# Performance work log

Measured on AMD Instinct MI355X. Metric: run time of the kernel, lower is better.

The kernel has to match this reference:

```python
import jax, jax.numpy as jnp
import numpy as np

# Production-scale dims
B = 256        # graphs per batch
NPG = 500      # nodes per graph (equal-size graphs; k<=NPG so no padding branch)
N = B * NPG    # 128000 total nodes
F = 128        # num_node_feats
D = 32         # latent_dim
K = 30         # sort-pool k
L = 3          # num_layers
E = 2_048_000  # edges (avg degree 16)


def _mlp(x, wa, ba, wb, bb):
    # 2-layer MLP(in -> D -> D) with ReLU between layers (standard GIN-style MLP)
    return jax.nn.relu(x @ wa + ba) @ wb + bb


def setup_inputs() -> dict:
    key = jax.random.key(0)
    ks = jax.random.split(key, 10)
    s = 0.05
    return {
        "node_feat": jax.random.normal(ks[0], (N, F), jnp.float32),
        "alpha": jax.random.normal(ks[1], (L + 1,), jnp.float32) * 0.5,
        "w0a": jax.random.normal(ks[2], (F, D), jnp.float32) * s,
        "b0a": jnp.zeros((D,), jnp.float32),
        "w0b": jax.random.normal(ks[3], (D, D), jnp.float32) * s,
        "b0b": jnp.zeros((D,), jnp.float32),
        "W1a": jax.random.normal(ks[4], (L, 3 * D, D), jnp.float32) * s,
        "B1a": jnp.zeros((L, D), jnp.float32),
        "W1b": jax.random.normal(ks[5], (L, D, D), jnp.float32) * s,
        "B1b": jnp.zeros((L, D), jnp.float32),
        "edge_src": jax.random.randint(ks[6], (E,), 0, N, jnp.int32),
        "edge_dst": jax.random.randint(ks[7], (E,), 0, N, jnp.int32),
    }


def reference(node_feat, alpha, w0a, b0a, w0b, b0b, W1a, B1a, W1b, B1b,
              edge_src, edge_dst):
    # --- aggregate_combine ---
    ego = _mlp(node_feat, w0a, b0a, w0b, b0b)            # [N, D]
    out = alpha[0] * ego
    for l in range(L):
        # gnn_spmm(n2n_sp, ego): binary adjacency SpMM == scatter-add over edges
        neig = jax.ops.segment_sum(ego[edge_src], edge_dst, num_segments=N)  # [N, D]
        agg = jnp.concatenate([ego, neig, neig + ego], axis=1)               # [N, 3D]
        ego = _mlp(agg, W1a[l], B1a[l], W1b[l], B1b[l])                      # [N, D]
        out = out + alpha[l + 1] * ego
    # --- per-graph sort pooling on wl_color = last channel of final ego ---
    wl_color = ego[:, -1].reshape(B, NPG)                # [B, NPG]
    _, idx = jax.lax.top_k(wl_color, K)                  # [B, K] local indices
    gidx = (idx + jnp.arange(B, dtype=idx.dtype)[:, None] * NPG).reshape(-1)
    sort_graphs = out[gidx].reshape(B, K * D)            # [B, k*latent_dim]
    return jax.nn.relu(sort_graphs)
```

## Files before the change

kernel.cpp:

```cpp
#include <hip/hip_runtime.h>
#include <math.h>

#define N_NODES 128000
#define B_G 256
#define NPG 500
#define F_IN 128
#define D_LAT 32
#define K_TOP 30
#define L_LAYERS 3
#define E_EDGES 2048000

#define BSH 7
#define NB (N_NODES >> BSH)
#define CHUNK 8192
#define CBLOCKS (E_EDGES / CHUNK)

__global__ __launch_bounds__(256) void k_mlp0(
    const float* __restrict__ X, const float* __restrict__ w0a,
    const float* __restrict__ b0a, const float* __restrict__ w0b,
    const float* __restrict__ b0b, const float* __restrict__ alpha,
    float* __restrict__ ego, float* __restrict__ outb)
{
    __shared__ float sWa[F_IN * D_LAT];
    __shared__ float sWb[D_LAT * D_LAT];
    __shared__ float sBa[D_LAT], sBb[D_LAT];

    const int t = threadIdx.x;
    for (int i = t; i < F_IN * D_LAT / 4; i += 256)
        ((float4*)sWa)[i] = ((const float4*)w0a)[i];
    for (int i = t; i < D_LAT * D_LAT / 4; i += 256)
        ((float4*)sWb)[i] = ((const float4*)w0b)[i];
    if (t < D_LAT) { sBa[t] = b0a[t]; sBb[t] = b0b[t]; }

    const size_t row = (size_t)blockIdx.x * 256 + t;
    const float4* xp = (const float4*)(X + row * F_IN);
    const float a0 = alpha[0];
    __syncthreads();

    float acc[D_LAT];
    #pragma unroll
    for (int d = 0; d < D_LAT; ++d) acc[d] = sBa[d];

    #pragma unroll
    for (int c = 0; c < F_IN / 16; ++c) {
        float4 x4[4];
        #pragma unroll
        for (int q = 0; q < 4; ++q) x4[q] = xp[c * 4 + q];
        #pragma unroll
        for (int q = 0; q < 4; ++q) {
            const float xs[4] = {x4[q].x, x4[q].y, x4[q].z, x4[q].w};
            #pragma unroll
            for (int ff = 0; ff < 4; ++ff) {
                const float xf = xs[ff];
                const float4* wr = (const float4*)(sWa + (c * 16 + q * 4 + ff) * D_LAT);
                #pragma unroll
                for (int dq = 0; dq < D_LAT / 4; ++dq) {
                    const float4 w = wr[dq];
                    acc[dq * 4 + 0] = fmaf(xf, w.x, acc[dq * 4 + 0]);
                    acc[dq * 4 + 1] = fmaf(xf, w.y, acc[dq * 4 + 1]);
                    acc[dq * 4 + 2] = fmaf(xf, w.z, acc[dq * 4 + 2]);
                    acc[dq * 4 + 3] = fmaf(xf, w.w, acc[dq * 4 + 3]);
                }
            }
        }
    }

    float acc2[D_LAT];
    #pragma unroll
    for (int d = 0; d < D_LAT; ++d) acc2[d] = sBb[d];
    #pragma unroll
    for (int dd = 0; dd < D_LAT; ++dd) {
        const float h = fmaxf(acc[dd], 0.f);
        const float4* wr = (const float4*)(sWb + dd * D_LAT);
        #pragma unroll
        for (int dq = 0; dq < D_LAT / 4; ++dq) {
            const float4 w = wr[dq];
            acc2[dq * 4 + 0] = fmaf(h, w.x, acc2[dq * 4 + 0]);
            acc2[dq * 4 + 1] = fmaf(h, w.y, acc2[dq * 4 + 1]);
            acc2[dq * 4 + 2] = fmaf(h, w.z, acc2[dq * 4 + 2]);
            acc2[dq * 4 + 3] = fmaf(h, w.w, acc2[dq * 4 + 3]);
        }
    }

    float4* eo = (float4*)(ego + row * D_LAT);
    float4* oo = (float4*)(outb + row * D_LAT);
    #pragma unroll
    for (int dq = 0; dq < D_LAT / 4; ++dq) {
        eo[dq] = make_float4(acc2[dq*4], acc2[dq*4+1], acc2[dq*4+2], acc2[dq*4+3]);
        oo[dq] = make_float4(a0*acc2[dq*4], a0*acc2[dq*4+1], a0*acc2[dq*4+2], a0*acc2[dq*4+3]);
    }
}

__global__ __launch_bounds__(256) void k_bcount(
    const int* __restrict__ edst, int* __restrict__ ghist)
{
    __shared__ int cnt[NB];
    const int t = threadIdx.x;
    for (int i = t; i < NB; i += 256) cnt[i] = 0;
    __syncthreads();
    const int ebase = blockIdx.x * CHUNK;
    for (int i = 0; i < CHUNK / 256; ++i)
        atomicAdd(&cnt[edst[ebase + i * 256 + t] >> BSH], 1);
    __syncthreads();
    for (int i = t; i < NB; i += 256)
        if (cnt[i]) atomicAdd(&ghist[i], cnt[i]);
}

__global__ __launch_bounds__(1024) void k_bscan(
    const int* __restrict__ ghist, int* __restrict__ gbase,
    int* __restrict__ gcursor)
{
    __shared__ int buf[2][1024];
    const int t = threadIdx.x;
    const int v = (t < NB) ? ghist[t] : 0;
    buf[0][t] = v;
    __syncthreads();
    int cur = 0;
    for (int o = 1; o < 1024; o <<= 1) {
        int x = buf[cur][t];
        if (t >= o) x += buf[cur][t - o];
        buf[cur ^ 1][t] = x;
        cur ^= 1;
        __syncthreads();
    }
    if (t < NB) { const int e = buf[cur][t] - v; gbase[t] = e; gcursor[t] = e; }
    if (t == 0) gbase[NB] = E_EDGES;
}

__global__ __launch_bounds__(256) void k_bscatter(
    const int* __restrict__ esrc, const int* __restrict__ edst,
    int* __restrict__ gcursor, int* __restrict__ packed)
{
    __shared__ int cnt[NB];
    __shared__ int sbase[NB];
    const int t = threadIdx.x;
    for (int i = t; i < NB; i += 256) cnt[i] = 0;
    __syncthreads();
    const int ebase = blockIdx.x * CHUNK;
    for (int i = 0; i < CHUNK / 256; ++i)
        atomicAdd(&cnt[edst[ebase + i * 256 + t] >> BSH], 1);
    __syncthreads();
    for (int i = t; i < NB; i += 256) {
        const int c = cnt[i];
        sbase[i] = c ? atomicAdd(&gcursor[i], c) : 0;
        cnt[i] = 0;
    }
    __syncthreads();
    for (int i = 0; i < CHUNK / 256; ++i) {
        const int e = ebase + i * 256 + t;
        const int d = edst[e], s = esrc[e];
        const int b = d >> BSH;
        const int r = atomicAdd(&cnt[b], 1);
        packed[sbase[b] + r] = (s << BSH) | (d & ((1 << BSH) - 1));
    }
}

__global__ __launch_bounds__(256) void k_bcsr(
    const int* __restrict__ gbase, const int* __restrict__ packed,
    int* __restrict__ off, int* __restrict__ srcidx)
{
    __shared__ int cnt[128];
    __shared__ int scn[128];
    __shared__ int sbuf[4096];
    const int b = blockIdx.x, t = threadIdx.x;
    const int s0 = gbase[b], s1 = gbase[b + 1], m = s1 - s0;

    if (t < 128) cnt[t] = 0;
    __syncthreads();
    for (int i = t; i < m; i += 256)
        atomicAdd(&cnt[packed[s0 + i] & 127], 1);
    __syncthreads();
    if (t == 0) {
        int a = 0;
        for (int k = 0; k < 128; ++k) { scn[k] = a; a += cnt[k]; }
    }
    __syncthreads();
    if (t < 128) { off[(b << BSH) + t] = s0 + scn[t]; cnt[t] = 0; }
    if (b == 0 && t == 0) off[N_NODES] = E_EDGES;
    __syncthreads();
    for (int i = t; i < m; i += 256) {
        const int p = packed[s0 + i];
        const int dl = p & 127;
        const int r = atomicAdd(&cnt[dl], 1);
        sbuf[scn[dl] + r] = p >> BSH;
    }
    __syncthreads();
    for (int i = t; i < m; i += 256) srcidx[s0 + i] = sbuf[i];
}

__global__ __launch_bounds__(256) void k_gather(
    const float* __restrict__ ego, const int* __restrict__ off,
    const int* __restrict__ srcidx, float* __restrict__ neig)
{
    const int t = threadIdx.x;
    const int node = blockIdx.x * 32 + (t >> 3);
    const int c = (t & 7) * 4;
    const int s0 = off[node], s1 = off[node + 1];
    float4 acc = {0.f, 0.f, 0.f, 0.f};
    for (int i = s0; i < s1; ++i) {
        const int s = srcidx[i];
        const float4 v = *(const float4*)(ego + (size_t)s * D_LAT + c);
        acc.x += v.x; acc.y += v.y; acc.z += v.z; acc.w += v.w;
    }
    *(float4*)(neig + (size_t)node * D_LAT + c) = acc;
}

__global__ __launch_bounds__(256) void k_mlp1(
    const float* __restrict__ ego_in, const float* __restrict__ neig,
    const float* __restrict__ W1a_l, const float* __restrict__ B1a_l,
    const float* __restrict__ W1b_l, const float* __restrict__ B1b_l,
    const float* __restrict__ alpha, const int l,
    float* __restrict__ ego_out, float* __restrict__ outb)
{
    __shared__ float sWe[D_LAT * D_LAT], sWn[D_LAT * D_LAT], sWb[D_LAT * D_LAT];
    __shared__ float sBa[D_LAT], sBb[D_LAT];

    const int t = threadIdx.x;
    for (int i = t; i < D_LAT * D_LAT; i += 256) {
        const float wc = W1a_l[2 * D_LAT * D_LAT + i];
        sWe[i] = W1a_l[i] + wc;
        sWn[i] = W1a_l[D_LAT * D_LAT + i] + wc;
        sWb[i] = W1b_l[i];
    }
    if (t < D_LAT) { sBa[t] = B1a_l[t]; sBb[t] = B1b_l[t]; }

    const size_t row = (size_t)blockIdx.x * 256 + t;
    const float4* ep = (const float4*)(ego_in + row * D_LAT);
    const float4* np_ = (const float4*)(neig + row * D_LAT);
    const float al = alpha[l + 1];
    __syncthreads();

    float acc[D_LAT];
    #pragma unroll
    for (int d = 0; d < D_LAT; ++d) acc[d] = sBa[d];

    #pragma unroll
    for (int c = 0; c < D_LAT / 4; ++c) {
        const float4 e4 = ep[c];
        const float4 n4 = np_[c];
        const float es[4] = {e4.x, e4.y, e4.z, e4.w};
        const float ns[4] = {n4.x, n4.y, n4.z, n4.w};
        #pragma unroll
        for (int ff = 0; ff < 4; ++ff) {
            const float fe = es[ff], fn = ns[ff];
            const float4* we = (const float4*)(sWe + (c * 4 + ff) * D_LAT);
            const float4* wn = (const float4*)(sWn + (c * 4 + ff) * D_LAT);
            #pragma unroll
            for (int dq = 0; dq < D_LAT / 4; ++dq) {
                const float4 a = we[dq], b = wn[dq];
                acc[dq * 4 + 0] = fmaf(fe, a.x, fmaf(fn, b.x, acc[dq * 4 + 0]));
                acc[dq * 4 + 1] = fmaf(fe, a.y, fmaf(fn, b.y, acc[dq * 4 + 1]));
                acc[dq * 4 + 2] = fmaf(fe, a.z, fmaf(fn, b.z, acc[dq * 4 + 2]));
                acc[dq * 4 + 3] = fmaf(fe, a.w, fmaf(fn, b.w, acc[dq * 4 + 3]));
            }
        }
    }

    float acc2[D_LAT];
    #pragma unroll
    for (int d = 0; d < D_LAT; ++d) acc2[d] = sBb[d];
    #pragma unroll
    for (int dd = 0; dd < D_LAT; ++dd) {
        const float h = fmaxf(acc[dd], 0.f);
        const float4* wr = (const float4*)(sWb + dd * D_LAT);
        #pragma unroll
        for (int dq = 0; dq < D_LAT / 4; ++dq) {
            const float4 w = wr[dq];
            acc2[dq * 4 + 0] = fmaf(h, w.x, acc2[dq * 4 + 0]);
            acc2[dq * 4 + 1] = fmaf(h, w.y, acc2[dq * 4 + 1]);
            acc2[dq * 4 + 2] = fmaf(h, w.z, acc2[dq * 4 + 2]);
            acc2[dq * 4 + 3] = fmaf(h, w.w, acc2[dq * 4 + 3]);
        }
    }

    float4* eo = (float4*)(ego_out + row * D_LAT);
    float4* oo = (float4*)(outb + row * D_LAT);
    #pragma unroll
    for (int dq = 0; dq < D_LAT / 4; ++dq) {
        const float4 prev = oo[dq];
        eo[dq] = make_float4(acc2[dq*4], acc2[dq*4+1], acc2[dq*4+2], acc2[dq*4+3]);
        oo[dq] = make_float4(fmaf(al, acc2[dq*4], prev.x),
                             fmaf(al, acc2[dq*4+1], prev.y),
                             fmaf(al, acc2[dq*4+2], prev.z),
                             fmaf(al, acc2[dq*4+3], prev.w));
    }
}

__global__ __launch_bounds__(256) void k_topk(
    const float* __restrict__ ego, const float* __restrict__ outb,
    float* __restrict__ y)
{
    __shared__ float vals[512];
    __shared__ int topidx[K_TOP];
    __shared__ float wv[4];
    __shared__ int wi[4];

    const int g = blockIdx.x, t = threadIdx.x;
    for (int i = t; i < 512; i += 256)
        vals[i] = (i < NPG) ? ego[((size_t)g * NPG + i) * D_LAT + (D_LAT - 1)]
                            : -INFINITY;
    __syncthreads();

    for (int k = 0; k < K_TOP; ++k) {
        float v = -INFINITY; int bi = 0x7fffffff;
        for (int i = t; i < NPG; i += 256) {
            const float x = vals[i];
            if (x > v || (x == v && i < bi)) { v = x; bi = i; }
        }
        for (int off = 32; off > 0; off >>= 1) {
            const float ov = __shfl_down(v, off);
            const int   oi = __shfl_down(bi, off);
            if (ov > v || (ov == v && oi < bi)) { v = ov; bi = oi; }
        }
        if ((t & 63) == 0) { wv[t >> 6] = v; wi[t >> 6] = bi; }
        __syncthreads();
        if (t == 0) {
            for (int w = 1; w < 4; ++w)
                if (wv[w] > v || (wv[w] == v && wi[w] < bi)) { v = wv[w]; bi = wi[w]; }
            topidx[k] = bi;
            vals[bi] = -INFINITY;
        }
        __syncthreads();
    }

    for (int j = t; j < K_TOP * D_LAT; j += 256) {
        const int kk = j >> 5, d = j & 31;
        const size_t node = (size_t)g * NPG + topidx[kk];
        y[(size_t)g * (K_TOP * D_LAT) + j] = fmaxf(outb[node * D_LAT + d], 0.f);
    }
}

extern "C" void kernel_launch(void* const* d_in, const int* in_sizes, int n_in,
                              void* d_out, int out_size, void* d_ws, size_t ws_size,
                              hipStream_t stream)
{
    const float* X    = (const float*)d_in[0];
    const float* alpha= (const float*)d_in[1];
    const float* w0a  = (const float*)d_in[2];
    const float* b0a  = (const float*)d_in[3];
    const float* w0b  = (const float*)d_in[4];
    const float* b0b  = (const float*)d_in[5];
    const float* W1a  = (const float*)d_in[6];
    const float* B1a  = (const float*)d_in[7];
    const float* W1b  = (const float*)d_in[8];
    const float* B1b  = (const float*)d_in[9];
    const int* esrc   = (const int*)d_in[10];
    const int* edst   = (const int*)d_in[11];
    float* y = (float*)d_out;

    float* ego    = (float*)d_ws;
    float* outb   = ego  + (size_t)N_NODES * D_LAT;
    float* neig   = outb + (size_t)N_NODES * D_LAT;
    int*   packed = (int*)neig;
    int*   off    = (int*)(neig + (size_t)N_NODES * D_LAT);
    int*   srcidx = off + (N_NODES + 1);
    int*   ghist  = srcidx + E_EDGES;
    int*   gbase  = ghist + NB;
    int*   gcursor= gbase + (NB + 1);

    hipMemsetAsync(ghist, 0, NB * sizeof(int), stream);
    k_bcount  <<<CBLOCKS, 256, 0, stream>>>(edst, ghist);
    k_bscan   <<<1, 1024, 0, stream>>>(ghist, gbase, gcursor);
    k_bscatter<<<CBLOCKS, 256, 0, stream>>>(esrc, edst, gcursor, packed);
    k_bcsr    <<<NB, 256, 0, stream>>>(gbase, packed, off, srcidx);

    k_mlp0<<<N_NODES / 256, 256, 0, stream>>>(X, w0a, b0a, w0b, b0b, alpha, ego, outb);

    for (int l = 0; l < L_LAYERS; ++l) {
        k_gather<<<N_NODES / 32, 256, 0, stream>>>(ego, off, srcidx, neig);
        k_mlp1<<<N_NODES / 256, 256, 0, stream>>>(
            ego, neig, W1a + (size_t)l * 96 * 32, B1a + (size_t)l * 32,
            W1b + (size_t)l * 32 * 32, B1b + (size_t)l * 32, alpha, l, ego, outb);
    }

    k_topk<<<B_G, 256, 0, stream>>>(ego, outb, y);
}
```

Baseline: 509.8 us.

## Split each node's MLP across two threads with shuffle reduction

The MLP kernels now assign two threads per node. In the first layer each thread handles half of the input features, and the partial sums are combined with a lane shuffle. In the second layer each thread computes half of the output columns. This doubles the thread count and halves per-thread register pressure, which should raise occupancy and improve latency hiding. In exchange it adds shuffles and redundant ReLU work, and each thread now issues narrower per-row memory accesses.

```diff
diff --git a/kernel.cpp b/kernel.cpp
--- a/kernel.cpp
+++ b/kernel.cpp
@@ -32,62 +32,67 @@
         ((float4*)sWb)[i] = ((const float4*)w0b)[i];
     if (t < D_LAT) { sBa[t] = b0a[t]; sBb[t] = b0b[t]; }
 
-    const size_t row = (size_t)blockIdx.x * 256 + t;
-    const float4* xp = (const float4*)(X + row * F_IN);
+    const int gtid = blockIdx.x * 256 + t;
+    const size_t row = (size_t)(gtid >> 1);
+    const int half = gtid & 1;
+    const float4* xp = (const float4*)(X + row * F_IN + half * 64);
+    const float* wbase = sWa + half * 64 * D_LAT;
     const float a0 = alpha[0];
     __syncthreads();
 
     float acc[D_LAT];
     #pragma unroll
-    for (int d = 0; d < D_LAT; ++d) acc[d] = sBa[d];
-
-    #pragma unroll
-    for (int c = 0; c < F_IN / 16; ++c) {
-        float4 x4[4];
+    for (int d = 0; d < D_LAT; ++d) acc[d] = 0.f;
+
+    #pragma unroll 1
+    for (int c = 0; c < 8; ++c) {
+        const float4 xa = xp[c * 2], xb = xp[c * 2 + 1];
+        const float xs[8] = {xa.x, xa.y, xa.z, xa.w, xb.x, xb.y, xb.z, xb.w};
         #pragma unroll
-        for (int q = 0; q < 4; ++q) x4[q] = xp[c * 4 + q];
+        for (int ff = 0; ff < 8; ++ff) {
+            const float xf = xs[ff];
+            const float4* wr = (const float4*)(wbase + (c * 8 + ff) * D_LAT);
+            #pragma unroll
+            for (int dq = 0; dq < D_LAT / 4; ++dq) {
+                const float4 w = wr[dq];
+                acc[dq * 4 + 0] = fmaf(xf, w.x, acc[dq * 4 + 0]);
+                acc[dq * 4 + 1] = fmaf(xf, w.y, acc[dq * 4 + 1]);
+                acc[dq * 4 + 2] = fmaf(xf, w.z, acc[dq * 4 + 2]);
+                acc[dq * 4 + 3] = fmaf(xf, w.w, acc[dq * 4 + 3]);
+            }
+        }
+    }
+
+    float h[D_LAT];
+    #pragma unroll
+    for (int d = 0; d < D_LAT; ++d) {
+        const float s = acc[d] + __shfl_xor(acc[d], 1);
+        h[d] = fmaxf(s + sBa[d], 0.f);
+    }
+
+    float acc2[16];
+    #pragma unroll
+    for (int j = 0; j < 16; ++j) acc2[j] = sBb[half * 16 + j];
+    #pragma unroll
+    for (int dd = 0; dd < D_LAT; ++dd) {
+        const float hd = h[dd];
+        const float4* wr = (const float4*)(sWb + dd * D_LAT + half * 16);
         #pragma unroll
         for (int q = 0; q < 4; ++q) {
-            const float xs[4] = {x4[q].x, x4[q].y, x4[q].z, x4[q].w};
-            #pragma unroll
-            for (int ff = 0; ff < 4; ++ff) {
-                const float xf = xs[ff];
-                const float4* wr = (const float4*)(sWa + (c * 16 + q * 4 + ff) * D_LAT);
-                #pragma unroll
-                for (int dq = 0; dq < D_LAT / 4; ++dq) {
-                    const float4 w = wr[dq];
-                    acc[dq * 4 + 0] = fmaf(xf, w.x, acc[dq * 4 + 0]);
-                    acc[dq * 4 + 1] = fmaf(xf, w.y, acc[dq * 4 + 1]);
-                    acc[dq * 4 + 2] = fmaf(xf, w.z, acc[dq * 4 + 2]);
-                    acc[dq * 4 + 3] = fmaf(xf, w.w, acc[dq * 4 + 3]);
-                }
-            }
-        }
-    }
-
-    float acc2[D_LAT];
-    #pragma unroll
-    for (int d = 0; d < D_LAT; ++d) acc2[d] = sBb[d];
-    #pragma unroll
-    for (int dd = 0; dd < D_LAT; ++dd) {
-        const float h = fmaxf(acc[dd], 0.f);
-        const float4* wr = (const float4*)(sWb + dd * D_LAT);
-        #pragma unroll
-        for (int dq = 0; dq < D_LAT / 4; ++dq) {
-            const float4 w = wr[dq];
-            acc2[dq * 4 + 0] = fmaf(h, w.x, acc2[dq * 4 + 0]);
-            acc2[dq * 4 + 1] = fmaf(h, w.y, acc2[dq * 4 + 1]);
-            acc2[dq * 4 + 2] = fmaf(h, w.z, acc2[dq * 4 + 2]);
-            acc2[dq * 4 + 3] = fmaf(h, w.w, acc2[dq * 4 + 3]);
-        }
-    }
-
-    float4* eo = (float4*)(ego + row * D_LAT);
-    float4* oo = (float4*)(outb + row * D_LAT);
-    #pragma unroll
-    for (int dq = 0; dq < D_LAT / 4; ++dq) {
-        eo[dq] = make_float4(acc2[dq*4], acc2[dq*4+1], acc2[dq*4+2], acc2[dq*4+3]);
-        oo[dq] = make_float4(a0*acc2[dq*4], a0*acc2[dq*4+1], a0*acc2[dq*4+2], a0*acc2[dq*4+3]);
+            const float4 w = wr[q];
+            acc2[q * 4 + 0] = fmaf(hd, w.x, acc2[q * 4 + 0]);
+            acc2[q * 4 + 1] = fmaf(hd, w.y, acc2[q * 4 + 1]);
+            acc2[q * 4 + 2] = fmaf(hd, w.z, acc2[q * 4 + 2]);
+            acc2[q * 4 + 3] = fmaf(hd, w.w, acc2[q * 4 + 3]);
+        }
+    }
+
+    float4* eo = (float4*)(ego + row * D_LAT + half * 16);
+    float4* oo = (float4*)(outb + row * D_LAT + half * 16);
+    #pragma unroll
+    for (int q = 0; q < 4; ++q) {
+        eo[q] = make_float4(acc2[q*4], acc2[q*4+1], acc2[q*4+2], acc2[q*4+3]);
+        oo[q] = make_float4(a0*acc2[q*4], a0*acc2[q*4+1], a0*acc2[q*4+2], a0*acc2[q*4+3]);
     }
 }
 
@@ -224,65 +229,71 @@
     }
     if (t < D_LAT) { sBa[t] = B1a_l[t]; sBb[t] = B1b_l[t]; }
 
-    const size_t row = (size_t)blockIdx.x * 256 + t;
-    const float4* ep = (const float4*)(ego_in + row * D_LAT);
-    const float4* np_ = (const float4*)(neig + row * D_LAT);
+    const int gtid = blockIdx.x * 256 + t;
+    const size_t row = (size_t)(gtid >> 1);
+    const int half = gtid & 1;
+    const float4* ip = (const float4*)((half ? neig : ego_in) + row * D_LAT);
+    const float* wbase = half ? sWn : sWe;
     const float al = alpha[l + 1];
     __syncthreads();
 
     float acc[D_LAT];
     #pragma unroll
-    for (int d = 0; d < D_LAT; ++d) acc[d] = sBa[d];
-
-    #pragma unroll
-    for (int c = 0; c < D_LAT / 4; ++c) {
-        const float4 e4 = ep[c];
-        const float4 n4 = np_[c];
-        const float es[4] = {e4.x, e4.y, e4.z, e4.w};
-        const float ns[4] = {n4.x, n4.y, n4.z, n4.w};
+    for (int d = 0; d < D_LAT; ++d) acc[d] = 0.f;
+
+    #pragma unroll 1
+    for (int c = 0; c < 4; ++c) {
+        const float4 xa = ip[c * 2], xb = ip[c * 2 + 1];
+        const float xs[8] = {xa.x, xa.y, xa.z, xa.w, xb.x, xb.y, xb.z, xb.w};
         #pragma unroll
-        for (int ff = 0; ff < 4; ++ff) {
-            const float fe = es[ff], fn = ns[ff];
-            const float4* we = (const float4*)(sWe + (c * 4 + ff) * D_LAT);
-            const float4* wn = (const float4*)(sWn + (c * 4 + ff) * D_LAT);
+        for (int ff = 0; ff < 8; ++ff) {
+            const float xf = xs[ff];
+            const float4* wr = (const float4*)(wbase + (c * 8 + ff) * D_LAT);
             #pragma unroll
             for (int dq = 0; dq < D_LAT / 4; ++dq) {
-                const float4 a = we[dq], b = wn[dq];
-                acc[dq * 4 + 0] = fmaf(fe, a.x, fmaf(fn, b.x, acc[dq * 4 + 0]));
-                acc[dq * 4 + 1] = fmaf(fe, a.y, fmaf(fn, b.y, acc[dq * 4 + 1]));
-                acc[dq * 4 + 2] = fmaf(fe, a.z, fmaf(fn, b.z, acc[dq * 4 + 2]));
-                acc[dq * 4 + 3] = fmaf(fe, a.w, fmaf(fn, b.w, acc[dq * 4 + 3]));
+                const float4 w = wr[dq];
+                acc[dq * 4 + 0] = fmaf(xf, w.x, acc[dq * 4 + 0]);
+                acc[dq * 4 + 1] = fmaf(xf, w.y, acc[dq * 4 + 1]);
+                acc[dq * 4 + 2] = fmaf(xf, w.z, acc[dq * 4 + 2]);
+                acc[dq * 4 + 3] = fmaf(xf, w.w, acc[dq * 4 + 3]);
             }
         }
     }
 
-    float acc2[D_LAT];
-    #pragma unroll
-    for (int d = 0; d < D_LAT; ++d) acc2[d] = sBb[d];
+    float h[D_LAT];
+    #pragma unroll
+    for (int d = 0; d < D_LAT; ++d) {
+        const float s = acc[d] + __shfl_xor(acc[d], 1);
+        h[d] = fmaxf(s + sBa[d], 0.f);
+    }
+
+    float acc2[16];
+    #pragma unroll
+    for (int j = 0; j < 16; ++j) acc2[j] = sBb[half * 16 + j];
     #pragma unroll
     for (int dd = 0; dd < D_LAT; ++dd) {
-        const float h = fmaxf(acc[dd], 0.f);
-        const float4* wr = (const float4*)(sWb + dd * D_LAT);
+        const float hd = h[dd];
+        const float4* wr = (const float4*)(sWb + dd * D_LAT + half * 16);
         #pragma unroll
-        for (int dq = 0; dq < D_LAT / 4; ++dq) {
-            const float4 w = wr[dq];
-            acc2[dq * 4 + 0] = fmaf(h, w.x, acc2[dq * 4 + 0]);
-            acc2[dq * 4 + 1] = fmaf(h, w.y, acc2[dq * 4 + 1]);
-            acc2[dq * 4 + 2] = fmaf(h, w.z, acc2[dq * 4 + 2]);
-            acc2[dq * 4 + 3] = fmaf(h, w.w, acc2[dq * 4 + 3]);
-        }
-    }
-
-    float4* eo = (float4*)(ego_out + row * D_LAT);
-    float4* oo = (float4*)(outb + row * D_LAT);
-    #pragma unroll
-    for (int dq = 0; dq < D_LAT / 4; ++dq) {
-        const float4 prev = oo[dq];
-        eo[dq] = make_float4(acc2[dq*4], acc2[dq*4+1], acc2[dq*4+2], acc2[dq*4+3]);
-        oo[dq] = make_float4(fmaf(al, acc2[dq*4], prev.x),
-                             fmaf(al, acc2[dq*4+1], prev.y),
-                             fmaf(al, acc2[dq*4+2], prev.z),
-                             fmaf(al, acc2[dq*4+3], prev.w));
+        for (int q = 0; q < 4; ++q) {
+            const float4 w = wr[q];
+            acc2[q * 4 + 0] = fmaf(hd, w.x, acc2[q * 4 + 0]);
+            acc2[q * 4 + 1] = fmaf(hd, w.y, acc2[q * 4 + 1]);
+            acc2[q * 4 + 2] = fmaf(hd, w.z, acc2[q * 4 + 2]);
+            acc2[q * 4 + 3] = fmaf(hd, w.w, acc2[q * 4 + 3]);
+        }
+    }
+
+    float4* eo = (float4*)(ego_out + row * D_LAT + half * 16);
+    float4* oo = (float4*)(outb + row * D_LAT + half * 16);
+    #pragma unroll
+    for (int q = 0; q < 4; ++q) {
+        const float4 prev = oo[q];
+        eo[q] = make_float4(acc2[q*4], acc2[q*4+1], acc2[q*4+2], acc2[q*4+3]);
+        oo[q] = make_float4(fmaf(al, acc2[q*4], prev.x),
+                            fmaf(al, acc2[q*4+1], prev.y),
+                            fmaf(al, acc2[q*4+2], prev.z),
+                            fmaf(al, acc2[q*4+3], prev.w));
     }
 }
 
@@ -364,11 +375,11 @@
     k_bscatter<<<CBLOCKS, 256, 0, stream>>>(esrc, edst, gcursor, packed);
     k_bcsr    <<<NB, 256, 0, stream>>>(gbase, packed, off, srcidx);
 
-    k_mlp0<<<N_NODES / 256, 256, 0, stream>>>(X, w0a, b0a, w0b, b0b, alpha, ego, outb);
+    k_mlp0<<<N_NODES * 2 / 256, 256, 0, stream>>>(X, w0a, b0a, w0b, b0b, alpha, ego, outb);
 
     for (int l = 0; l < L_LAYERS; ++l) {
         k_gather<<<N_NODES / 32, 256, 0, stream>>>(ego, off, srcidx, neig);
-        k_mlp1<<<N_NODES / 256, 256, 0, stream>>>(
+        k_mlp1<<<N_NODES * 2 / 256, 256, 0, stream>>>(
             ego, neig, W1a + (size_t)l * 96 * 32, B1a + (size_t)l * 32,
             W1b + (size_t)l * 32 * 32, B1b + (size_t)l * 32, alpha, l, ego, outb);
     }
```

After: 469.3 us. -8.0%, faster.

## Fuse neighbor gather into per-layer MLP kernel with ping-pong buffers and scalar weight loads

Applied to the files above, without the earlier changes.

Merges the per-layer gather and MLP kernels into one kernel where each thread gathers its node's neighbor sum (all 32 channels) and then runs the MLP, double-buffering ego between layers. The folded W1a weights are precomputed once by a small kernel, and the MLPs now read weights directly from global memory as uniform scalar loads instead of staging them in LDS. This removes the neig round-trip through memory and one launch per layer. In exchange, the gather becomes one thread per node with 128-byte row reads and a serial edge loop, so accesses are less coalesced and load is imbalanced across lanes.

```diff
diff --git a/kernel.cpp b/kernel.cpp
--- a/kernel.cpp
+++ b/kernel.cpp
@@ -15,79 +15,74 @@
 #define CHUNK 8192
 #define CBLOCKS (E_EDGES / CHUNK)
 
+__global__ __launch_bounds__(256) void k_foldw(
+    const float* __restrict__ W1a, float* __restrict__ wfold)
+{
+    const int l = blockIdx.x, t = threadIdx.x;
+    const float* base = W1a + (size_t)l * 3 * D_LAT * D_LAT;
+    float* o = wfold + (size_t)l * 2 * D_LAT * D_LAT;
+    for (int i = t; i < D_LAT * D_LAT; i += 256) {
+        const float wc = base[2 * D_LAT * D_LAT + i];
+        o[i] = base[i] + wc;
+        o[D_LAT * D_LAT + i] = base[D_LAT * D_LAT + i] + wc;
+    }
+}
+
 __global__ __launch_bounds__(256) void k_mlp0(
     const float* __restrict__ X, const float* __restrict__ w0a,
     const float* __restrict__ b0a, const float* __restrict__ w0b,
     const float* __restrict__ b0b, const float* __restrict__ alpha,
     float* __restrict__ ego, float* __restrict__ outb)
 {
-    __shared__ float sWa[F_IN * D_LAT];
-    __shared__ float sWb[D_LAT * D_LAT];
-    __shared__ float sBa[D_LAT], sBb[D_LAT];
-
-    const int t = threadIdx.x;
-    for (int i = t; i < F_IN * D_LAT / 4; i += 256)
-        ((float4*)sWa)[i] = ((const float4*)w0a)[i];
-    for (int i = t; i < D_LAT * D_LAT / 4; i += 256)
-        ((float4*)sWb)[i] = ((const float4*)w0b)[i];
-    if (t < D_LAT) { sBa[t] = b0a[t]; sBb[t] = b0b[t]; }
-
-    const size_t row = (size_t)blockIdx.x * 256 + t;
+    const size_t row = (size_t)blockIdx.x * 256 + threadIdx.x;
     const float4* xp = (const float4*)(X + row * F_IN);
     const float a0 = alpha[0];
-    __syncthreads();
 
     float acc[D_LAT];
     #pragma unroll
-    for (int d = 0; d < D_LAT; ++d) acc[d] = sBa[d];
-
-    #pragma unroll
+    for (int j = 0; j < D_LAT; ++j) acc[j] = b0a[j];
+
+    #pragma unroll 1
     for (int c = 0; c < F_IN / 16; ++c) {
-        float4 x4[4];
-        #pragma unroll
-        for (int q = 0; q < 4; ++q) x4[q] = xp[c * 4 + q];
-        #pragma unroll
-        for (int q = 0; q < 4; ++q) {
-            const float xs[4] = {x4[q].x, x4[q].y, x4[q].z, x4[q].w};
+        const float4 x0 = xp[c * 4 + 0], x1 = xp[c * 4 + 1];
+        const float4 x2 = xp[c * 4 + 2], x3 = xp[c * 4 + 3];
+        const float xs[16] = {x0.x, x0.y, x0.z, x0.w, x1.x, x1.y, x1.z, x1.w,
+                              x2.x, x2.y, x2.z, x2.w, x3.x, x3.y, x3.z, x3.w};
+        #pragma unroll
+        for (int ff = 0; ff < 16; ++ff) {
+            const float xf = xs[ff];
+            const float* wr = w0a + (c * 16 + ff) * D_LAT;
             #pragma unroll
-            for (int ff = 0; ff < 4; ++ff) {
-                const float xf = xs[ff];
-                const float4* wr = (const float4*)(sWa + (c * 16 + q * 4 + ff) * D_LAT);
-                #pragma unroll
-                for (int dq = 0; dq < D_LAT / 4; ++dq) {
-                    const float4 w = wr[dq];
-                    acc[dq * 4 + 0] = fmaf(xf, w.x, acc[dq * 4 + 0]);
-                    acc[dq * 4 + 1] = fmaf(xf, w.y, acc[dq * 4 + 1]);
-                    acc[dq * 4 + 2] = fmaf(xf, w.z, acc[dq * 4 + 2]);
-                    acc[dq * 4 + 3] = fmaf(xf, w.w, acc[dq * 4 + 3]);
-                }
-            }
-        }
-    }
+            for (int j = 0; j < D_LAT; ++j)
+                acc[j] = fmaf(xf, wr[j], acc[j]);
+        }
+    }
+
+    #pragma unroll
+    for (int j = 0; j < D_LAT; ++j) acc[j] = fmaxf(acc[j], 0.f);
 
     float acc2[D_LAT];
     #pragma unroll
-    for (int d = 0; d < D_LAT; ++d) acc2[d] = sBb[d];
-    #pragma unroll
-    for (int dd = 0; dd < D_LAT; ++dd) {
-        const float h = fmaxf(acc[dd], 0.f);
-        const float4* wr = (const float4*)(sWb + dd * D_LAT);
-        #pragma unroll
-        for (int dq = 0; dq < D_LAT / 4; ++dq) {
-            const float4 w = wr[dq];
-            acc2[dq * 4 + 0] = fmaf(h, w.x, acc2[dq * 4 + 0]);
-            acc2[dq * 4 + 1] = fmaf(h, w.y, acc2[dq * 4 + 1]);
-            acc2[dq * 4 + 2] = fmaf(h, w.z, acc2[dq * 4 + 2]);
-            acc2[dq * 4 + 3] = fmaf(h, w.w, acc2[dq * 4 + 3]);
+    for (int j = 0; j < D_LAT; ++j) acc2[j] = b0b[j];
+    #pragma unroll 1
+    for (int c = 0; c < D_LAT / 8; ++c) {
+        #pragma unroll
+        for (int kk = 0; kk < 8; ++kk) {
+            const float h = acc[c * 8 + kk];
+            const float* wr = w0b + (c * 8 + kk) * D_LAT;
+            #pragma unroll
+            for (int j = 0; j < D_LAT; ++j)
+                acc2[j] = fmaf(h, wr[j], acc2[j]);
         }
     }
 
     float4* eo = (float4*)(ego + row * D_LAT);
     float4* oo = (float4*)(outb + row * D_LAT);
     #pragma unroll
-    for (int dq = 0; dq < D_LAT / 4; ++dq) {
-        eo[dq] = make_float4(acc2[dq*4], acc2[dq*4+1], acc2[dq*4+2], acc2[dq*4+3]);
-        oo[dq] = make_float4(a0*acc2[dq*4], a0*acc2[dq*4+1], a0*acc2[dq*4+2], a0*acc2[dq*4+3]);
+    for (int q = 0; q < D_LAT / 4; ++q) {
+        eo[q] = make_float4(acc2[q*4], acc2[q*4+1], acc2[q*4+2], acc2[q*4+3]);
+        oo[q] = make_float4(a0*acc2[q*4], a0*acc2[q*4+1],
+                            a0*acc2[q*4+2], a0*acc2[q*4+3]);
     }
 }
 
@@ -188,101 +183,92 @@
     for (int i = t; i < m; i += 256) srcidx[s0 + i] = sbuf[i];
 }
 
-__global__ __launch_bounds__(256) void k_gather(
-    const float* __restrict__ ego, const int* __restrict__ off,
-    const int* __restrict__ srcidx, float* __restrict__ neig)
-{
-    const int t = threadIdx.x;
-    const int node = blockIdx.x * 32 + (t >> 3);
-    const int c = (t & 7) * 4;
-    const int s0 = off[node], s1 = off[node + 1];
-    float4 acc = {0.f, 0.f, 0.f, 0.f};
+__global__ __launch_bounds__(256) void k_layer(
+    const float* __restrict__ in, const int* __restrict__ off,
+    const int* __restrict__ srcidx, const float* __restrict__ wfold_l,
+    const float* __restrict__ W1b_l, const float* __restrict__ B1a_l,
+    const float* __restrict__ B1b_l, const float* __restrict__ alpha,
+    const int l, float* __restrict__ out, float* __restrict__ outb)
+{
+    const size_t n = (size_t)blockIdx.x * 256 + threadIdx.x;
+    const int s0 = off[n], s1 = off[n + 1];
+    const float al = alpha[l + 1];
+
+    float4 ng4[D_LAT / 4];
+    #pragma unroll
+    for (int q = 0; q < D_LAT / 4; ++q) ng4[q] = make_float4(0.f, 0.f, 0.f, 0.f);
+    int s = (s0 < s1) ? srcidx[s0] : 0;
     for (int i = s0; i < s1; ++i) {
-        const int s = srcidx[i];
-        const float4 v = *(const float4*)(ego + (size_t)s * D_LAT + c);
-        acc.x += v.x; acc.y += v.y; acc.z += v.z; acc.w += v.w;
-    }
-    *(float4*)(neig + (size_t)node * D_LAT + c) = acc;
-}
-
-__global__ __launch_bounds__(256) void k_mlp1(
-    const float* __restrict__ ego_in, const float* __restrict__ neig,
-    const float* __restrict__ W1a_l, const float* __restrict__ B1a_l,
-    const float* __restrict__ W1b_l, const float* __restrict__ B1b_l,
-    const float* __restrict__ alpha, const int l,
-    float* __restrict__ ego_out, float* __restrict__ outb)
-{
-    __shared__ float sWe[D_LAT * D_LAT], sWn[D_LAT * D_LAT], sWb[D_LAT * D_LAT];
-    __shared__ float sBa[D_LAT], sBb[D_LAT];
-
-    const int t = threadIdx.x;
-    for (int i = t; i < D_LAT * D_LAT; i += 256) {
-        const float wc = W1a_l[2 * D_LAT * D_LAT + i];
-        sWe[i] = W1a_l[i] + wc;
-        sWn[i] = W1a_l[D_LAT * D_LAT + i] + wc;
-        sWb[i] = W1b_l[i];
-    }
-    if (t < D_LAT) { sBa[t] = B1a_l[t]; sBb[t] = B1b_l[t]; }
-
-    const size_t row = (size_t)blockIdx.x * 256 + t;
-    const float4* ep = (const float4*)(ego_in + row * D_LAT);
-    const float4* np_ = (const float4*)(neig + row * D_LAT);
-    const float al = alpha[l + 1];
-    __syncthreads();
+        const int snext = (i + 1 < s1) ? srcidx[i + 1] : 0;
+        const float4* vp = (const float4*)(in + (size_t)s * D_LAT);
+        #pragma unroll
+        for (int q = 0; q < D_LAT / 4; ++q) {
+            const float4 v = vp[q];
+            ng4[q].x += v.x; ng4[q].y += v.y; ng4[q].z += v.z; ng4[q].w += v.w;
+        }
+        s = snext;
+    }
+    float ngs[D_LAT];
+    #pragma unroll
+    for (int q = 0; q < D_LAT / 4; ++q) {
+        ngs[q*4] = ng4[q].x; ngs[q*4+1] = ng4[q].y;
+        ngs[q*4+2] = ng4[q].z; ngs[q*4+3] = ng4[q].w;
+    }
+
+    float eg[D_LAT];
+    {
+        const float4* ep = (const float4*)(in + n * D_LAT);
+        #pragma unroll
+        for (int q = 0; q < D_LAT / 4; ++q) {
+            const float4 v = ep[q];
+            eg[q*4] = v.x; eg[q*4+1] = v.y; eg[q*4+2] = v.z; eg[q*4+3] = v.w;
+        }
+    }
 
     float acc[D_LAT];
     #pragma unroll
-    for (int d = 0; d < D_LAT; ++d) acc[d] = sBa[d];
-
-    #pragma unroll
-    for (int c = 0; c < D_LAT / 4; ++c) {
-        const float4 e4 = ep[c];
-        const float4 n4 = np_[c];
-        const float es[4] = {e4.x, e4.y, e4.z, e4.w};
-        const float ns[4] = {n4.x, n4.y, n4.z, n4.w};
-        #pragma unroll
-        for (int ff = 0; ff < 4; ++ff) {
-            const float fe = es[ff], fn = ns[ff];
-            const float4* we = (const float4*)(sWe + (c * 4 + ff) * D_LAT);
-            const float4* wn = (const float4*)(sWn + (c * 4 + ff) * D_LAT);
+    for (int j = 0; j < D_LAT; ++j) acc[j] = B1a_l[j];
+    #pragma unroll 1
+    for (int c = 0; c < D_LAT / 8; ++c) {
+        #pragma unroll
+        for (int kk = 0; kk < 8; ++kk) {
+            const int k = c * 8 + kk;
+            const float fe = eg[k], fn = ngs[k];
+            const float* we = wfold_l + k * D_LAT;
+            const float* wn = wfold_l + D_LAT * D_LAT + k * D_LAT;
             #pragma unroll
-            for (int dq = 0; dq < D_LAT / 4; ++dq) {
-                const float4 a = we[dq], b = wn[dq];
-                acc[dq * 4 + 0] = fmaf(fe, a.x, fmaf(fn, b.x, acc[dq * 4 + 0]));
-                acc[dq * 4 + 1] = fmaf(fe, a.y, fmaf(fn, b.y, acc[dq * 4 + 1]));
-                acc[dq * 4 + 2] = fmaf(fe, a.z, fmaf(fn, b.z, acc[dq * 4 + 2]));
-                acc[dq * 4 + 3] = fmaf(fe, a.w, fmaf(fn, b.w, acc[dq * 4 + 3]));
-            }
-        }
-    }
+            for (int j = 0; j < D_LAT; ++j)
+                acc[j] = fmaf(fe, we[j], fmaf(fn, wn[j], acc[j]));
+        }
+    }
+    #pragma unroll
+    for (int j = 0; j < D_LAT; ++j) acc[j] = fmaxf(acc[j], 0.f);
 
     float acc2[D_LAT];
     #pragma unroll
-    for (int d = 0; d < D_LAT; ++d) acc2[d] = sBb[d];
-    #pragma unroll
-    for (int dd = 0; dd < D_LAT; ++dd) {
-        const float h = fmaxf(acc[dd], 0.f);
-        const float4* wr = (const float4*)(sWb + dd * D_LAT);
-        #pragma unroll
-        for (int dq = 0; dq < D_LAT / 4; ++dq) {
-            const float4 w = wr[dq];
-            acc2[dq * 4 + 0] = fmaf(h, w.x, acc2[dq * 4 + 0]);
-            acc2[dq * 4 + 1] = fmaf(h, w.y, acc2[dq * 4 + 1]);
-            acc2[dq * 4 + 2] = fmaf(h, w.z, acc2[dq * 4 + 2]);
-            acc2[dq * 4 + 3] = fmaf(h, w.w, acc2[dq * 4 + 3]);
-        }
-    }
-
-    float4* eo = (float4*)(ego_out + row * D_LAT);
-    float4* oo = (float4*)(outb + row * D_LAT);
-    #pragma unroll
-    for (int dq = 0; dq < D_LAT / 4; ++dq) {
-        const float4 prev = oo[dq];
-        eo[dq] = make_float4(acc2[dq*4], acc2[dq*4+1], acc2[dq*4+2], acc2[dq*4+3]);
-        oo[dq] = make_float4(fmaf(al, acc2[dq*4], prev.x),
-                             fmaf(al, acc2[dq*4+1], prev.y),
-                             fmaf(al, acc2[dq*4+2], prev.z),
-                             fmaf(al, acc2[dq*4+3], prev.w));
+    for (int j = 0; j < D_LAT; ++j) acc2[j] = B1b_l[j];
+    #pragma unroll 1
+    for (int c = 0; c < D_LAT / 8; ++c) {
+        #pragma unroll
+        for (int kk = 0; kk < 8; ++kk) {
+            const float h = acc[c * 8 + kk];
+            const float* wr = W1b_l + (c * 8 + kk) * D_LAT;
+            #pragma unroll
+            for (int j = 0; j < D_LAT; ++j)
+                acc2[j] = fmaf(h, wr[j], acc2[j]);
+        }
+    }
+
+    float4* eo = (float4*)(out + n * D_LAT);
+    float4* oo = (float4*)(outb + n * D_LAT);
+    #pragma unroll
+    for (int q = 0; q < D_LAT / 4; ++q) {
+        const float4 prev = oo[q];
+        eo[q] = make_float4(acc2[q*4], acc2[q*4+1], acc2[q*4+2], acc2[q*4+3]);
+        oo[q] = make_float4(fmaf(al, acc2[q*4], prev.x),
+                            fmaf(al, acc2[q*4+1], prev.y),
+                            fmaf(al, acc2[q*4+2], prev.z),
+                            fmaf(al, acc2[q*4+3], prev.w));
     }
 }
 
@@ -348,15 +334,18 @@
     const int* edst   = (const int*)d_in[11];
     float* y = (float*)d_out;
 
-    float* ego    = (float*)d_ws;
-    float* outb   = ego  + (size_t)N_NODES * D_LAT;
-    float* neig   = outb + (size_t)N_NODES * D_LAT;
-    int*   packed = (int*)neig;
-    int*   off    = (int*)(neig + (size_t)N_NODES * D_LAT);
+    float* egoA   = (float*)d_ws;
+    float* outb   = egoA + (size_t)N_NODES * D_LAT;
+    float* egoB   = outb + (size_t)N_NODES * D_LAT;
+    int*   packed = (int*)egoB;
+    int*   off    = (int*)(egoB + (size_t)N_NODES * D_LAT);
     int*   srcidx = off + (N_NODES + 1);
     int*   ghist  = srcidx + E_EDGES;
     int*   gbase  = ghist + NB;
     int*   gcursor= gbase + (NB + 1);
+    float* wfold  = (float*)(gcursor + NB);
+
+    k_foldw<<<L_LAYERS, 256, 0, stream>>>(W1a, wfold);
 
     hipMemsetAsync(ghist, 0, NB * sizeof(int), stream);
     k_bcount  <<<CBLOCKS, 256, 0, stream>>>(edst, ghist);
@@ -364,14 +353,17 @@
     k_bscatter<<<CBLOCKS, 256, 0, stream>>>(esrc, edst, gcursor, packed);
     k_bcsr    <<<NB, 256, 0, stream>>>(gbase, packed, off, srcidx);
 
-    k_mlp0<<<N_NODES / 256, 256, 0, stream>>>(X, w0a, b0a, w0b, b0b, alpha, ego, outb);
-
+    k_mlp0<<<N_NODES / 256, 256, 0, stream>>>(X, w0a, b0a, w0b, b0b, alpha, egoA, outb);
+
+    float* cur = egoA;
+    float* nxt = egoB;
     for (int l = 0; l < L_LAYERS; ++l) {
-        k_gather<<<N_NODES / 32, 256, 0, stream>>>(ego, off, srcidx, neig);
-        k_mlp1<<<N_NODES / 256, 256, 0, stream>>>(
-            ego, neig, W1a + (size_t)l * 96 * 32, B1a + (size_t)l * 32,
-            W1b + (size_t)l * 32 * 32, B1b + (size_t)l * 32, alpha, l, ego, outb);
-    }
-
-    k_topk<<<B_G, 256, 0, stream>>>(ego, outb, y);
-}
+        k_layer<<<N_NODES / 256, 256, 0, stream>>>(
+            cur, off, srcidx, wfold + (size_t)l * 2 * D_LAT * D_LAT,
+            W1b + (size_t)l * D_LAT * D_LAT, B1a + (size_t)l * D_LAT,
+            B1b + (size_t)l * D_LAT, alpha, l, nxt, outb);
+        float* tmp = cur; cur = nxt; nxt = tmp;
+    }
+
+    k_topk<<<B_G, 256, 0, stream>>>(cur, outb, y);
+}
```

Measured after the change: 430.8 us. -15.5%, faster.
